# Optimization experiments

Measured on AMD Instinct MI355X. Metric: run time of the kernel, lower is better.

The kernel has to match this reference:

```python
import jax, jax.numpy as jnp
import numpy as np

N, D, H, TOPK = 1024, 128, 8, 16
HD = D // H
EPS = 1e-5


def _linear_init(key, fan_in, fan_out):
    lim = 1.0 / np.sqrt(fan_in)
    kw, kb = jax.random.split(key)
    W = jax.random.uniform(kw, (fan_in, fan_out), minval=-lim, maxval=lim, dtype=jnp.float32)
    b = jax.random.uniform(kb, (fan_out,), minval=-lim, maxval=lim, dtype=jnp.float32)
    return W, b


def setup_inputs() -> dict:
    key = jax.random.key(0)
    ks = jax.random.split(key, 16)
    h = jax.random.normal(ks[0], (N, D), dtype=jnp.float32)
    e = jax.random.normal(ks[1], (N, N, D), dtype=jnp.float32)
    adjm_bin = jax.random.randint(ks[2], (N, N), 0, 2, dtype=jnp.int32)
    Wq, bq = _linear_init(ks[3], D, D)
    Wk, bk = _linear_init(ks[4], D, D)
    Wv, bv = _linear_init(ks[5], D, D)
    We, be = _linear_init(ks[6], D, H)
    Wo, bo = _linear_init(ks[7], D, D)
    Wf1, bf1 = _linear_init(ks[8], D, 4 * D)
    Wf2, bf2 = _linear_init(ks[9], 4 * D, D)
    # torch LSTMCell layout: W_ih [4D, D], W_hh [4D, D], gate order i,f,g,o
    lim = 1.0 / np.sqrt(D)
    Wih = jax.random.uniform(ks[10], (4 * D, D), minval=-lim, maxval=lim, dtype=jnp.float32)
    Whh = jax.random.uniform(ks[11], (4 * D, D), minval=-lim, maxval=lim, dtype=jnp.float32)
    bih = jax.random.uniform(ks[12], (4 * D,), minval=-lim, maxval=lim, dtype=jnp.float32)
    bhh = jax.random.uniform(ks[13], (4 * D,), minval=-lim, maxval=lim, dtype=jnp.float32)
    gn_g = jnp.ones((D,), jnp.float32); gn_b = jnp.zeros((D,), jnp.float32)
    ln1_g = jnp.ones((D,), jnp.float32); ln1_b = jnp.zeros((D,), jnp.float32)
    ln2_g = jnp.ones((D,), jnp.float32); ln2_b = jnp.zeros((D,), jnp.float32)
    return dict(h=h, e=e, adjm_bin=adjm_bin, Wq=Wq, bq=bq, Wk=Wk, bk=bk, Wv=Wv, bv=bv,
                We=We, be=be, Wo=Wo, bo=bo, Wf1=Wf1, bf1=bf1, Wf2=Wf2, bf2=bf2,
                Wih=Wih, Whh=Whh, bih=bih, bhh=bhh, gn_g=gn_g, gn_b=gn_b,
                ln1_g=ln1_g, ln1_b=ln1_b, ln2_g=ln2_g, ln2_b=ln2_b)


def _layernorm(x, g, b):
    mu = jnp.mean(x, axis=-1, keepdims=True)
    var = jnp.var(x, axis=-1, keepdims=True)
    return g * (x - mu) * jax.lax.rsqrt(var + EPS) + b


def _forward(h, e, Wq, bq, Wk, bk, Wv, bv, We, be, Wo, bo, Wf1, bf1, Wf2, bf2,
             Wih, Whh, bih, bhh, gn_g, gn_b, ln1_g, ln1_b, ln2_g, ln2_b):
    n = h.shape[0]
    residual = h
    q = (h @ Wq + bq).reshape(n, H, HD)
    k = (h @ Wk + bk).reshape(n, H, HD)
    v = (h @ Wv + bv).reshape(n, H, HD)
    scores = jnp.einsum('ihd,jhd->ijh', q, k) / np.sqrt(HD).astype(np.float32)
    scores = scores + (e @ We + be)                      # [N, N, H]
    # per-head top-k over neighbor dim j (axis=1)
    s = scores.transpose(0, 2, 1)                        # [N, H, N]
    _, idx = jax.lax.top_k(s, TOPK)                      # [N, H, K]
    mask = jnp.zeros(s.shape, bool).at[
        jnp.arange(n)[:, None, None], jnp.arange(H)[None, :, None], idx].set(True)
    mask = mask.transpose(0, 2, 1)                       # [N, N, H]
    scores = jnp.where(mask, scores, -jnp.inf)
    attn = jax.nn.softmax(scores, axis=1)
    h_attn = jnp.einsum('ijh,jhd->ihd', attn, v).reshape(n, D)
    h_attn = h_attn @ Wo + bo
    x = _layernorm(residual + h_attn, ln1_g, ln1_b)
    # LSTMCell with zero initial state (memory_state=None branch)
    gates = x @ Wih.T + bih + jnp.zeros_like(x) @ Whh.T + bhh
    gi, gf, gg, go = jnp.split(gates, 4, axis=-1)
    i = jax.nn.sigmoid(gi); f = jax.nn.sigmoid(gf)
    g = jnp.tanh(gg); o = jax.nn.sigmoid(go)
    c_next = i * g                                       # f * 0 dropped
    h_next = o * jnp.tanh(c_next)
    x = x + h_next
    # GraphNorm: normalize over node dim 0
    mu = jnp.mean(x, axis=0, keepdims=True)
    var = jnp.var(x, axis=0, keepdims=True)
    x = gn_g * (x - mu) * jax.lax.rsqrt(var + EPS) + gn_b
    h_ffn = jax.nn.relu(x @ Wf1 + bf1) @ Wf2 + bf2
    out = _layernorm(x + h_ffn, ln2_g, ln2_b)
    return out, h_next, c_next


def reference(h, e, adjm_bin, Wq, bq, Wk, bk, Wv, bv, We, be, Wo, bo, Wf1, bf1,
              Wf2, bf2, Wih, Whh, bih, bhh, gn_g, gn_b, ln1_g, ln1_b, ln2_g, ln2_b):
    # adjm_bin is accepted but unused, matching the original forward
    return _forward(h, e, Wq, bq, Wk, bk, Wv, bv, We, be, Wo, bo, Wf1, bf1,
                    Wf2, bf2, Wih, Whh, bih, bhh, gn_g, gn_b, ln1_g, ln1_b,
                    ln2_g, ln2_b)
```

## Files before the change

### kernel.cpp

```cpp
#include <hip/hip_runtime.h>
#include <math.h>
#include <float.h>
#include <stdint.h>

#define NN 1024
#define DD 128
#define HH 8
#define HDIM 16
#define KTOP 16
#define SCP 1032

typedef float vf4 __attribute__((ext_vector_type(4)));

__device__ __forceinline__ float wred_sum(float v) {
#pragma unroll
  for (int off = 32; off > 0; off >>= 1) v += __shfl_xor(v, off, 64);
  return v;
}

__device__ __forceinline__ float4 ntload4(const float* p) {
  vf4 r = __builtin_nontemporal_load((const vf4*)p);
  return make_float4(r.x, r.y, r.z, r.w);
}

template <int CTRL>
__device__ __forceinline__ float dpp_add(float v) {
  int x = __builtin_amdgcn_update_dpp(0, __float_as_int(v), CTRL, 0xF, 0xF, true);
  return v + __int_as_float(x);
}
#define DPP_XOR1 0xB1
#define DPP_XOR2 0x4E
#define DPP_ROR4 0x124
#define DPP_ROR8 0x128

__global__ __launch_bounds__(128) void k_qkv(
    const float* __restrict__ h,
    const float* __restrict__ Wq, const float* __restrict__ bq,
    const float* __restrict__ Wk, const float* __restrict__ bk,
    const float* __restrict__ Wv, const float* __restrict__ bv,
    float* __restrict__ q, float* __restrict__ k, float* __restrict__ v) {
  __shared__ float hrow[4][DD];
  const int t = threadIdx.x;
  const int i0 = blockIdx.x * 4;
#pragma unroll
  for (int r = 0; r < 4; ++r) hrow[r][t] = h[(i0 + r) * DD + t];
  __syncthreads();
  const float* W[3] = {Wq, Wk, Wv};
  const float* B[3] = {bq, bk, bv};
  float* O[3] = {q, k, v};
#pragma unroll
  for (int m = 0; m < 3; ++m) {
    float a0 = 0.f, a1 = 0.f, a2 = 0.f, a3 = 0.f;
    const float* Wm = W[m];
#pragma unroll 8
    for (int c = 0; c < DD; ++c) {
      float w = Wm[c * DD + t];
      a0 += hrow[0][c] * w; a1 += hrow[1][c] * w;
      a2 += hrow[2][c] * w; a3 += hrow[3][c] * w;
    }
    float b = B[m][t];
    float* Om = O[m];
    Om[(i0 + 0) * DD + t] = a0 + b;
    Om[(i0 + 1) * DD + t] = a1 + b;
    Om[(i0 + 2) * DD + t] = a2 + b;
    Om[(i0 + 3) * DD + t] = a3 + b;
  }
}

__global__ __launch_bounds__(256) void k_qk(
    const float* __restrict__ q, const float* __restrict__ kk,
    const float* __restrict__ be, float* __restrict__ scG) {
  __shared__ float qs[16 * 64];
  __shared__ float ks[16 * 64];
  const int t = threadIdx.x;
  const int i0 = blockIdx.x * 64;
  const int j0 = blockIdx.y * 64;
  const int h = blockIdx.z;

  {
    const int il = t >> 2;
    const int dq = (t & 3) * 4;
    float4 qv = *(const float4*)(q + (size_t)(i0 + il) * DD + h * HDIM + dq);
    qs[(dq + 0) * 64 + il] = qv.x * 0.25f;
    qs[(dq + 1) * 64 + il] = qv.y * 0.25f;
    qs[(dq + 2) * 64 + il] = qv.z * 0.25f;
    qs[(dq + 3) * 64 + il] = qv.w * 0.25f;
    float4 kv = *(const float4*)(kk + (size_t)(j0 + il) * DD + h * HDIM + dq);
    ks[(dq + 0) * 64 + il] = kv.x;
    ks[(dq + 1) * 64 + il] = kv.y;
    ks[(dq + 2) * 64 + il] = kv.z;
    ks[(dq + 3) * 64 + il] = kv.w;
  }
  __syncthreads();

  const int ti = t & 15;
  const int tj = t >> 4;
  float acc[4][4] = {{0,0,0,0},{0,0,0,0},{0,0,0,0},{0,0,0,0}};
#pragma unroll
  for (int d = 0; d < 16; ++d) {
    float4 qv = *(const float4*)&qs[d * 64 + ti * 4];
    float4 kv = *(const float4*)&ks[d * 64 + tj * 4];
    acc[0][0] += qv.x * kv.x; acc[0][1] += qv.x * kv.y; acc[0][2] += qv.x * kv.z; acc[0][3] += qv.x * kv.w;
    acc[1][0] += qv.y * kv.x; acc[1][1] += qv.y * kv.y; acc[1][2] += qv.y * kv.z; acc[1][3] += qv.y * kv.w;
    acc[2][0] += qv.z * kv.x; acc[2][1] += qv.z * kv.y; acc[2][2] += qv.z * kv.z; acc[2][3] += qv.z * kv.w;
    acc[3][0] += qv.w * kv.x; acc[3][1] += qv.w * kv.y; acc[3][2] += qv.w * kv.z; acc[3][3] += qv.w * kv.w;
  }
  const float beh = be[h];
#pragma unroll
  for (int a = 0; a < 4; ++a) {
    float4 st = make_float4(acc[a][0] + beh, acc[a][1] + beh,
                            acc[a][2] + beh, acc[a][3] + beh);
    *(float4*)(scG + (size_t)(i0 + ti * 4 + a) * (HH * NN) + h * NN + j0 + tj * 4) = st;
  }
}

__global__ __launch_bounds__(128, 2) void k_attn(
    const float* __restrict__ e, const float* __restrict__ We,
    const float* __restrict__ scG, const float* __restrict__ v,
    float* __restrict__ hattn) {
  __shared__ float sc[HH * SCP];
  const int tid = threadIdx.x;
  const int lane = tid & 63;
  const int wv = tid >> 6;
  const int i = blockIdx.x;

  const int lrow = lane >> 4;
  const int c16 = lane & 15;
  const int c0 = c16 * 8;
  const int rb = wv * 8 + lrow;

  const float* ei = e + ((size_t)i << 17);
  const float* pa = ei + (size_t)rb * DD + c0;
  const float* pb = pa + 4 * DD;

  float4 ea0 = ntload4(pa);          float4 ea1 = ntload4(pa + 4);
  float4 eb0 = ntload4(pb);          float4 eb1 = ntload4(pb + 4);

  float4 w[16];
#pragma unroll
  for (int cl = 0; cl < 8; ++cl) {
    w[cl * 2]     = *(const float4*)(We + (c0 + cl) * HH);
    w[cl * 2 + 1] = *(const float4*)(We + (c0 + cl) * HH + 4);
  }

  {
    const float* scb = scG + (size_t)i * (HH * NN);
    for (int f = tid; f < 2048; f += 128) {
      int h = f >> 8, j4 = f & 255;
      *(float4*)&sc[h * SCP + j4 * 4] = *(const float4*)&scb[h * NN + j4 * 4];
    }
  }
  __syncthreads();

  for (int t = 0; t < 64; ++t) {
    float4 na0, na1, nb0, nb1;
    const bool more = (t + 1 < 64);
    if (more) {
      const float* xa = pa + (size_t)(t + 1) * (16 * DD);
      const float* xb = xa + 4 * DD;
      na0 = ntload4(xa);  na1 = ntload4(xa + 4);
      nb0 = ntload4(xb);  nb1 = ntload4(xb + 4);
    }

    float acca[8] = {0,0,0,0,0,0,0,0};
    float accb[8] = {0,0,0,0,0,0,0,0};
    const float eva[8] = {ea0.x, ea0.y, ea0.z, ea0.w, ea1.x, ea1.y, ea1.z, ea1.w};
    const float evb[8] = {eb0.x, eb0.y, eb0.z, eb0.w, eb1.x, eb1.y, eb1.z, eb1.w};
#pragma unroll
    for (int cl = 0; cl < 8; ++cl) {
      float4 wlo = w[cl * 2], whi = w[cl * 2 + 1];
      float a = eva[cl], b = evb[cl];
      acca[0] += a * wlo.x; acca[1] += a * wlo.y; acca[2] += a * wlo.z; acca[3] += a * wlo.w;
      acca[4] += a * whi.x; acca[5] += a * whi.y; acca[6] += a * whi.z; acca[7] += a * whi.w;
      accb[0] += b * wlo.x; accb[1] += b * wlo.y; accb[2] += b * wlo.z; accb[3] += b * wlo.w;
      accb[4] += b * whi.x; accb[5] += b * whi.y; accb[6] += b * whi.z; accb[7] += b * whi.w;
    }

#pragma unroll
    for (int hh = 0; hh < 8; ++hh) {
      acca[hh] = dpp_add<DPP_XOR1>(acca[hh]);
      acca[hh] = dpp_add<DPP_XOR2>(acca[hh]);
      acca[hh] = dpp_add<DPP_ROR4>(acca[hh]);
      acca[hh] = dpp_add<DPP_ROR8>(acca[hh]);
      accb[hh] = dpp_add<DPP_XOR1>(accb[hh]);
      accb[hh] = dpp_add<DPP_XOR2>(accb[hh]);
      accb[hh] = dpp_add<DPP_ROR4>(accb[hh]);
      accb[hh] = dpp_add<DPP_ROR8>(accb[hh]);
    }

    if ((c16 & 1) == 0) {
      const int h = c16 >> 1;
      float sa = acca[0], sb = accb[0];
#pragma unroll
      for (int hh = 1; hh < 8; ++hh) {
        if (h == hh) { sa = acca[hh]; sb = accb[hh]; }
      }
      const int j = t * 16 + rb;
      sc[h * SCP + j]     += sa;
      sc[h * SCP + j + 4] += sb;
    }

    if (more) { ea0 = na0; ea1 = na1; eb0 = nb0; eb1 = nb1; }
  }
  __syncthreads();

#pragma unroll 1
  for (int hp = 0; hp < 4; ++hp) {
    const int h = wv * 4 + hp;
    float val[16];
#pragma unroll
    for (int s = 0; s < 16; ++s) val[s] = sc[h * SCP + s * 64 + lane];
    int selj[16];
    float wgt[16];
    float vmax = 0.f, denom = 0.f;
#pragma unroll
    for (int t = 0; t < KTOP; ++t) {
      float bv = -FLT_MAX;
      int bj = 0x7FFFFFFF;
#pragma unroll
      for (int s = 0; s < 16; ++s) {
        float vs = val[s];
        int jj = s * 64 + lane;
        if (vs > bv) { bv = vs; bj = jj; }
      }
#pragma unroll
      for (int off = 32; off > 0; off >>= 1) {
        float ov = __shfl_xor(bv, off, 64);
        int oj = __shfl_xor(bj, off, 64);
        if (ov > bv || (ov == bv && oj < bj)) { bv = ov; bj = oj; }
      }
      selj[t] = bj;
      if (t == 0) vmax = bv;
      float wexp = expf(bv - vmax);
      wgt[t] = wexp;
      denom += wexp;
      const int so = bj >> 6;
      if ((bj & 63) == lane) {
#pragma unroll
        for (int s = 0; s < 16; ++s)
          if (s == so) val[s] = -FLT_MAX;
      }
    }
    const float inv = 1.0f / denom;
    const int d = lane & 15;
    float acc = 0.f;
#pragma unroll
    for (int t = 0; t < KTOP; ++t)
      acc += wgt[t] * v[(size_t)selj[t] * DD + h * HDIM + d];
    if (lane < 16) hattn[i * DD + h * HDIM + d] = acc * inv;
  }
}

__global__ __launch_bounds__(128) void k_post1(
    const float* __restrict__ h, const float* __restrict__ hattn,
    const float* __restrict__ Wo, const float* __restrict__ bo,
    const float* __restrict__ Wih, const float* __restrict__ bih, const float* __restrict__ bhh,
    const float* __restrict__ ln1g, const float* __restrict__ ln1b,
    float* __restrict__ x2, float* __restrict__ outh, float* __restrict__ outc) {
  __shared__ float arow[4][DD];
  __shared__ float x1s[4][DD];
  __shared__ float redS[4][2], redQ[4][2];
  const int t = threadIdx.x;
  const int i0 = blockIdx.x * 4;
#pragma unroll
  for (int r = 0; r < 4; ++r) arow[r][t] = hattn[(i0 + r) * DD + t];
  __syncthreads();
  float o0 = 0.f, o1 = 0.f, o2 = 0.f, o3 = 0.f;
#pragma unroll 4
  for (int c = 0; c < DD; ++c) {
    float w = Wo[c * DD + t];
    o0 += arow[0][c] * w; o1 += arow[1][c] * w;
    o2 += arow[2][c] * w; o3 += arow[3][c] * w;
  }
  float ovals[4] = {o0, o1, o2, o3};
  const float bov = bo[t], g1 = ln1g[t], b1 = ln1b[t];
#pragma unroll
  for (int r = 0; r < 4; ++r) {
    float res = h[(i0 + r) * DD + t] + ovals[r] + bov;
    float s1 = wred_sum(res), s2 = wred_sum(res * res);
    if ((t & 63) == 0) { redS[r][t >> 6] = s1; redQ[r][t >> 6] = s2; }
    __syncthreads();
    float mu = (redS[r][0] + redS[r][1]) * (1.f / 128.f);
    float var = (redQ[r][0] + redQ[r][1]) * (1.f / 128.f) - mu * mu;
    x1s[r][t] = g1 * (res - mu) * rsqrtf(var + 1e-5f) + b1;
  }
  __syncthreads();
  float gi[4] = {0, 0, 0, 0}, gg[4] = {0, 0, 0, 0}, go[4] = {0, 0, 0, 0};
  for (int c = 0; c < DD; ++c) {
    float wI = Wih[(t)*DD + c];
    float wG = Wih[(t + 256) * DD + c];
    float wO = Wih[(t + 384) * DD + c];
#pragma unroll
    for (int r = 0; r < 4; ++r) {
      float xv = x1s[r][c];
      gi[r] += xv * wI; gg[r] += xv * wG; go[r] += xv * wO;
    }
  }
  const float biI = bih[t] + bhh[t];
  const float biG = bih[t + 256] + bhh[t + 256];
  const float biO = bih[t + 384] + bhh[t + 384];
#pragma unroll
  for (int r = 0; r < 4; ++r) {
    float iv = 1.f / (1.f + expf(-(gi[r] + biI)));
    float gv = tanhf(gg[r] + biG);
    float ov = 1.f / (1.f + expf(-(go[r] + biO)));
    float cn = iv * gv;
    float hn = ov * tanhf(cn);
    outh[(i0 + r) * DD + t] = hn;
    outc[(i0 + r) * DD + t] = cn;
    x2[(i0 + r) * DD + t] = x1s[r][t] + hn;
  }
}

__global__ __launch_bounds__(256) void k_gncol(const float* __restrict__ x2,
                                               float* __restrict__ pS, float* __restrict__ pQ) {
  const int t = threadIdx.x, b = blockIdx.x;
  const int c = t & 127, half = t >> 7;
  const int r0 = b * 16 + half * 8;
  float s = 0.f, qq = 0.f;
#pragma unroll
  for (int r = 0; r < 8; ++r) {
    float v = x2[(r0 + r) * DD + c];
    s += v; qq += v * v;
  }
  pS[(b * 2 + half) * DD + c] = s;
  pQ[(b * 2 + half) * DD + c] = qq;
}

__global__ __launch_bounds__(128) void k_gnfin(const float* __restrict__ pS,
                                               const float* __restrict__ pQ,
                                               float* __restrict__ stats) {
  const int c = threadIdx.x;
  float s = 0.f, qq = 0.f;
#pragma unroll 8
  for (int kk = 0; kk < 128; ++kk) { s += pS[kk * DD + c]; qq += pQ[kk * DD + c]; }
  float mu = s * (1.f / 1024.f);
  float var = qq * (1.f / 1024.f) - mu * mu;
  stats[c] = mu;
  stats[DD + c] = rsqrtf(var + 1e-5f);
}

__global__ __launch_bounds__(256) void k_ffn(
    const float* __restrict__ x2, const float* __restrict__ stats,
    const float* __restrict__ gng, const float* __restrict__ gnb,
    const float* __restrict__ Wf1, const float* __restrict__ bf1,
    const float* __restrict__ Wf2, const float* __restrict__ bf2,
    const float* __restrict__ ln2g, const float* __restrict__ ln2b,
    float* __restrict__ out) {
  __shared__ float x3s[4][DD];
  __shared__ float hid[4][512];
  __shared__ float redC[4][256];
  __shared__ float redS[4][4], redQ[4][4];
  const int t = threadIdx.x;
  const int i0 = blockIdx.x * 4;
  for (int idx = t; idx < 4 * DD; idx += 256) {
    int r = idx >> 7, c = idx & 127;
    float vv = x2[(i0 + r) * DD + c];
    x3s[r][c] = gng[c] * (vv - stats[c]) * stats[DD + c] + gnb[c];
  }
  __syncthreads();
  {
    float a0[4] = {0, 0, 0, 0}, a1[4] = {0, 0, 0, 0};
#pragma unroll 2
    for (int c = 0; c < DD; ++c) {
      float w1 = Wf1[c * 512 + t];
      float w2 = Wf1[c * 512 + t + 256];
#pragma unroll
      for (int r = 0; r < 4; ++r) {
        float xv = x3s[r][c];
        a0[r] += xv * w1; a1[r] += xv * w2;
      }
    }
    float bb1 = bf1[t], bb2 = bf1[t + 256];
#pragma unroll
    for (int r = 0; r < 4; ++r) {
      hid[r][t] = fmaxf(a0[r] + bb1, 0.f);
      hid[r][t + 256] = fmaxf(a1[r] + bb2, 0.f);
    }
  }
  __syncthreads();
  const int d = t & 127, half = t >> 7;
  {
    float a[4] = {0, 0, 0, 0};
    for (int uu = 0; uu < 256; ++uu) {
      int u = half * 256 + uu;
      float w = Wf2[u * DD + d];
#pragma unroll
      for (int r = 0; r < 4; ++r) a[r] += hid[r][u] * w;
    }
#pragma unroll
    for (int r = 0; r < 4; ++r) redC[r][t] = a[r];
  }
  __syncthreads();
  const int lane = t & 63, wvv = t >> 6;
#pragma unroll 1
  for (int r = 0; r < 4; ++r) {
    float z = 0.f;
    if (t < DD) z = x3s[r][t] + redC[r][t] + redC[r][t + 128] + bf2[t];
    float s1 = wred_sum(z), s2 = wred_sum(z * z);
    if (lane == 0) { redS[r][wvv] = s1; redQ[r][wvv] = s2; }
    __syncthreads();
    float sum = redS[r][0] + redS[r][1] + redS[r][2] + redS[r][3];
    float sq = redQ[r][0] + redQ[r][1] + redQ[r][2] + redQ[r][3];
    float mu = sum * (1.f / 128.f);
    float var = sq * (1.f / 128.f) - mu * mu;
    float rs = rsqrtf(var + 1e-5f);
    if (t < DD) out[(i0 + r) * DD + t] = ln2g[t] * (z - mu) * rs + ln2b[t];
  }
}

extern "C" void kernel_launch(void* const* d_in, const int* in_sizes, int n_in,
                              void* d_out, int out_size, void* d_ws, size_t ws_size,
                              hipStream_t stream) {
  const float* h   = (const float*)d_in[0];
  const float* e   = (const float*)d_in[1];
  const float* Wq  = (const float*)d_in[3];
  const float* bq  = (const float*)d_in[4];
  const float* Wk  = (const float*)d_in[5];
  const float* bk  = (const float*)d_in[6];
  const float* Wv  = (const float*)d_in[7];
  const float* bv  = (const float*)d_in[8];
  const float* We  = (const float*)d_in[9];
  const float* be  = (const float*)d_in[10];
  const float* Wo  = (const float*)d_in[11];
  const float* bo  = (const float*)d_in[12];
  const float* Wf1 = (const float*)d_in[13];
  const float* bf1 = (const float*)d_in[14];
  const float* Wf2 = (const float*)d_in[15];
  const float* bf2 = (const float*)d_in[16];
  const float* Wih = (const float*)d_in[17];
  const float* bih = (const float*)d_in[19];
  const float* bhh = (const float*)d_in[20];
  const float* gng = (const float*)d_in[21];
  const float* gnb = (const float*)d_in[22];
  const float* l1g = (const float*)d_in[23];
  const float* l1b = (const float*)d_in[24];
  const float* l2g = (const float*)d_in[25];
  const float* l2b = (const float*)d_in[26];

  float* W = (float*)d_ws;
  float* q     = W;
  float* k     = W + 131072;
  float* v     = W + 262144;
  float* hattn = W + 393216;
  float* x2    = W + 524288;
  float* stats = W + 655360;
  float* pS    = W + 655616;
  float* pQ    = W + 672000;
  float* scG   = W + 1048576;

  float* out  = (float*)d_out;
  float* outh = out + 131072;
  float* outc = out + 262144;

  hipLaunchKernelGGL(k_qkv, dim3(256), dim3(128), 0, stream,
                     h, Wq, bq, Wk, bk, Wv, bv, q, k, v);
  hipLaunchKernelGGL(k_qk, dim3(16, 16, 8), dim3(256), 0, stream,
                     q, k, be, scG);
  hipLaunchKernelGGL(k_attn, dim3(1024), dim3(128), 0, stream,
                     e, We, scG, v, hattn);
  hipLaunchKernelGGL(k_post1, dim3(256), dim3(128), 0, stream,
                     h, hattn, Wo, bo, Wih, bih, bhh, l1g, l1b, x2, outh, outc);
  hipLaunchKernelGGL(k_gncol, dim3(64), dim3(256), 0, stream, x2, pS, pQ);
  hipLaunchKernelGGL(k_gnfin, dim3(1), dim3(128), 0, stream, pS, pQ, stats);
  hipLaunchKernelGGL(k_ffn, dim3(256), dim3(256), 0, stream,
                     x2, stats, gng, gnb, Wf1, bf1, Wf2, bf2, l2g, l2b, out);
}
```

Baseline: 246.4 us.

## Split edge-score and top-k into separate kernels with interleaved streaming

The fused attention kernel is split in two. A new edge-score kernel streams the 512 MB e tensor with 2048 blocks, each covering 16-row chunks strided across the whole tensor, and adds the per-head edge bias directly into the global score buffer. A separate top-k/softmax kernel then reads the scores from global memory instead of LDS. The aim is more parallelism and better DRAM streaming for the bandwidth-bound e pass, at the cost of an extra kernel launch and a global read-modify-write of the score matrix.

```diff
diff --git a/kernel.cpp b/kernel.cpp
--- a/kernel.cpp
+++ b/kernel.cpp
@@ -8,7 +8,6 @@
 #define HH 8
 #define HDIM 16
 #define KTOP 16
-#define SCP 1032
 
 typedef float vf4 __attribute__((ext_vector_type(4)));
 
@@ -76,7 +75,6 @@
   const int i0 = blockIdx.x * 64;
   const int j0 = blockIdx.y * 64;
   const int h = blockIdx.z;
-
   {
     const int il = t >> 2;
     const int dq = (t & 3) * 4;
@@ -92,7 +90,6 @@
     ks[(dq + 3) * 64 + il] = kv.w;
   }
   __syncthreads();
-
   const int ti = t & 15;
   const int tj = t >> 4;
   float acc[4][4] = {{0,0,0,0},{0,0,0,0},{0,0,0,0},{0,0,0,0}};
@@ -114,68 +111,59 @@
   }
 }
 
-__global__ __launch_bounds__(128, 2) void k_attn(
+__global__ __launch_bounds__(128) void k_score(
     const float* __restrict__ e, const float* __restrict__ We,
-    const float* __restrict__ scG, const float* __restrict__ v,
-    float* __restrict__ hattn) {
-  __shared__ float sc[HH * SCP];
+    float* __restrict__ scG) {
   const int tid = threadIdx.x;
   const int lane = tid & 63;
   const int wv = tid >> 6;
-  const int i = blockIdx.x;
-
   const int lrow = lane >> 4;
   const int c16 = lane & 15;
-  const int c0 = c16 * 8;
-  const int rb = wv * 8 + lrow;
-
-  const float* ei = e + ((size_t)i << 17);
-  const float* pa = ei + (size_t)rb * DD + c0;
-  const float* pb = pa + 4 * DD;
-
-  float4 ea0 = ntload4(pa);          float4 ea1 = ntload4(pa + 4);
-  float4 eb0 = ntload4(pb);          float4 eb1 = ntload4(pb + 4);
-
-  float4 w[16];
-#pragma unroll
-  for (int cl = 0; cl < 8; ++cl) {
-    w[cl * 2]     = *(const float4*)(We + (c0 + cl) * HH);
-    w[cl * 2 + 1] = *(const float4*)(We + (c0 + cl) * HH + 4);
-  }
-
-  {
-    const float* scb = scG + (size_t)i * (HH * NN);
-    for (int f = tid; f < 2048; f += 128) {
-      int h = f >> 8, j4 = f & 255;
-      *(float4*)&sc[h * SCP + j4 * 4] = *(const float4*)&scb[h * NN + j4 * 4];
-    }
-  }
-  __syncthreads();
-
-  for (int t = 0; t < 64; ++t) {
-    float4 na0, na1, nb0, nb1;
-    const bool more = (t + 1 < 64);
+  const int cl0 = c16 * 4;
+  const int ra = wv * 8 + lrow;
+
+  float4 wlo[8], whi[8];
+#pragma unroll
+  for (int cl = 0; cl < 4; ++cl) {
+    wlo[cl * 2]     = *(const float4*)(We + (cl0 + cl) * HH);
+    wlo[cl * 2 + 1] = *(const float4*)(We + (cl0 + cl) * HH + 4);
+    whi[cl * 2]     = *(const float4*)(We + (64 + cl0 + cl) * HH);
+    whi[cl * 2 + 1] = *(const float4*)(We + (64 + cl0 + cl) * HH + 4);
+  }
+
+  const float* p0 = e + (((size_t)blockIdx.x) << 11) + (size_t)ra * DD + cl0;
+  float4 eaL = ntload4(p0),          eaH = ntload4(p0 + 64);
+  float4 ebL = ntload4(p0 + 4 * DD), ebH = ntload4(p0 + 4 * DD + 64);
+
+  for (int it = 0; it < 32; ++it) {
+    float4 naL, naH, nbL, nbH;
+    const bool more = (it + 1 < 32);
     if (more) {
-      const float* xa = pa + (size_t)(t + 1) * (16 * DD);
-      const float* xb = xa + 4 * DD;
-      na0 = ntload4(xa);  na1 = ntload4(xa + 4);
-      nb0 = ntload4(xb);  nb1 = ntload4(xb + 4);
+      const float* xa = p0 + (size_t)(it + 1) * 4194304ull;
+      naL = ntload4(xa);          naH = ntload4(xa + 64);
+      nbL = ntload4(xa + 4 * DD); nbH = ntload4(xa + 4 * DD + 64);
     }
 
     float acca[8] = {0,0,0,0,0,0,0,0};
     float accb[8] = {0,0,0,0,0,0,0,0};
-    const float eva[8] = {ea0.x, ea0.y, ea0.z, ea0.w, ea1.x, ea1.y, ea1.z, ea1.w};
-    const float evb[8] = {eb0.x, eb0.y, eb0.z, eb0.w, eb1.x, eb1.y, eb1.z, eb1.w};
-#pragma unroll
-    for (int cl = 0; cl < 8; ++cl) {
-      float4 wlo = w[cl * 2], whi = w[cl * 2 + 1];
-      float a = eva[cl], b = evb[cl];
-      acca[0] += a * wlo.x; acca[1] += a * wlo.y; acca[2] += a * wlo.z; acca[3] += a * wlo.w;
-      acca[4] += a * whi.x; acca[5] += a * whi.y; acca[6] += a * whi.z; acca[7] += a * whi.w;
-      accb[0] += b * wlo.x; accb[1] += b * wlo.y; accb[2] += b * wlo.z; accb[3] += b * wlo.w;
-      accb[4] += b * whi.x; accb[5] += b * whi.y; accb[6] += b * whi.z; accb[7] += b * whi.w;
-    }
-
+    const float eLa[4] = {eaL.x, eaL.y, eaL.z, eaL.w};
+    const float eHa[4] = {eaH.x, eaH.y, eaH.z, eaH.w};
+    const float eLb[4] = {ebL.x, ebL.y, ebL.z, ebL.w};
+    const float eHb[4] = {ebH.x, ebH.y, ebH.z, ebH.w};
+#pragma unroll
+    for (int cl = 0; cl < 4; ++cl) {
+      float4 wl0 = wlo[cl * 2], wl1 = wlo[cl * 2 + 1];
+      float4 wh0 = whi[cl * 2], wh1 = whi[cl * 2 + 1];
+      float al = eLa[cl], ah = eHa[cl], bl = eLb[cl], bh = eHb[cl];
+      acca[0] += al * wl0.x + ah * wh0.x; acca[1] += al * wl0.y + ah * wh0.y;
+      acca[2] += al * wl0.z + ah * wh0.z; acca[3] += al * wl0.w + ah * wh0.w;
+      acca[4] += al * wl1.x + ah * wh1.x; acca[5] += al * wl1.y + ah * wh1.y;
+      acca[6] += al * wl1.z + ah * wh1.z; acca[7] += al * wl1.w + ah * wh1.w;
+      accb[0] += bl * wl0.x + bh * wh0.x; accb[1] += bl * wl0.y + bh * wh0.y;
+      accb[2] += bl * wl0.z + bh * wh0.z; accb[3] += bl * wl0.w + bh * wh0.w;
+      accb[4] += bl * wl1.x + bh * wh1.x; accb[5] += bl * wl1.y + bh * wh1.y;
+      accb[6] += bl * wl1.z + bh * wh1.z; accb[7] += bl * wl1.w + bh * wh1.w;
+    }
 #pragma unroll
     for (int hh = 0; hh < 8; ++hh) {
       acca[hh] = dpp_add<DPP_XOR1>(acca[hh]);
@@ -188,28 +176,46 @@
       accb[hh] = dpp_add<DPP_ROR8>(accb[hh]);
     }
 
-    if ((c16 & 1) == 0) {
-      const int h = c16 >> 1;
+    const int gc = blockIdx.x + it * 2048;
+    const int i = gc >> 6;
+    const int j = ((gc & 63) << 4) + ra;
+    float* scb = scG + (size_t)i * (HH * NN);
+    const int sub = c16 & 3;
+    if (sub == 0) {
+      const int h = c16 >> 2;
       float sa = acca[0], sb = accb[0];
 #pragma unroll
-      for (int hh = 1; hh < 8; ++hh) {
-        if (h == hh) { sa = acca[hh]; sb = accb[hh]; }
-      }
-      const int j = t * 16 + rb;
-      sc[h * SCP + j]     += sa;
-      sc[h * SCP + j + 4] += sb;
-    }
-
-    if (more) { ea0 = na0; ea1 = na1; eb0 = nb0; eb1 = nb1; }
-  }
-  __syncthreads();
+      for (int hh = 1; hh < 4; ++hh) if (h == hh) { sa = acca[hh]; sb = accb[hh]; }
+      scb[h * NN + j]     += sa;
+      scb[h * NN + j + 4] += sb;
+    } else if (sub == 1) {
+      const int g = c16 >> 2;
+      float sa = acca[4], sb = accb[4];
+#pragma unroll
+      for (int hh = 1; hh < 4; ++hh) if (g == hh) { sa = acca[4 + hh]; sb = accb[4 + hh]; }
+      scb[(4 + g) * NN + j]     += sa;
+      scb[(4 + g) * NN + j + 4] += sb;
+    }
+
+    if (more) { eaL = naL; eaH = naH; ebL = nbL; ebH = nbH; }
+  }
+}
+
+__global__ __launch_bounds__(128) void k_topk(
+    const float* __restrict__ scG, const float* __restrict__ v,
+    float* __restrict__ hattn) {
+  const int tid = threadIdx.x;
+  const int lane = tid & 63;
+  const int wv = tid >> 6;
+  const int i = blockIdx.x;
+  const float* scb = scG + (size_t)i * (HH * NN);
 
 #pragma unroll 1
   for (int hp = 0; hp < 4; ++hp) {
     const int h = wv * 4 + hp;
     float val[16];
 #pragma unroll
-    for (int s = 0; s < 16; ++s) val[s] = sc[h * SCP + s * 64 + lane];
+    for (int s = 0; s < 16; ++s) val[s] = scb[h * NN + s * 64 + lane];
     int selj[16];
     float wgt[16];
     float vmax = 0.f, denom = 0.f;
@@ -457,8 +463,10 @@
                      h, Wq, bq, Wk, bk, Wv, bv, q, k, v);
   hipLaunchKernelGGL(k_qk, dim3(16, 16, 8), dim3(256), 0, stream,
                      q, k, be, scG);
-  hipLaunchKernelGGL(k_attn, dim3(1024), dim3(128), 0, stream,
-                     e, We, scG, v, hattn);
+  hipLaunchKernelGGL(k_score, dim3(2048), dim3(128), 0, stream,
+                     e, We, scG);
+  hipLaunchKernelGGL(k_topk, dim3(1024), dim3(128), 0, stream,
+                     scG, v, hattn);
   hipLaunchKernelGGL(k_post1, dim3(256), dim3(128), 0, stream,
                      h, hattn, Wo, bo, Wih, bih, bhh, l1g, l1b, x2, outh, outc);
   hipLaunchKernelGGL(k_gncol, dim3(64), dim3(256), 0, stream, x2, pS, pQ);
```

New measurement: 325.3 us. 1.32x slower.
